# Optimization experiments

Measured on AMD Instinct MI355X. Metric: run time of the kernel, lower is better.

The kernel has to match this reference:

```python
import jax, jax.numpy as jnp
import numpy as np

N, E = 50000, 600000
DIN, DMID, DATTR, DOUT, DEMB, DH, K = 128, 128, 32, 128, 256, 768, 16


def setup_inputs() -> dict:
    key = jax.random.key(0)
    ks = jax.random.split(key, 12)
    s = lambda d: 1.0 / np.sqrt(d)
    return {
        "x": jax.random.normal(ks[0], (N, DIN), jnp.float32),
        "attributes": jax.random.normal(ks[1], (N, DATTR), jnp.float32),
        "edge_weight": jax.random.uniform(ks[2], (E,), jnp.float32),
        "hidden_state": jax.random.normal(ks[3], (1, DH), jnp.float32),
        "edge_index": jax.random.randint(ks[4], (2, E), 0, N, jnp.int64),
        "W1": jax.random.normal(ks[5], (DIN, DMID), jnp.float32) * s(DIN),
        "b1": jnp.zeros((DMID,), jnp.float32),
        "W2": jax.random.normal(ks[6], (DMID + DATTR, DOUT), jnp.float32) * s(DMID + DATTR),
        "b2": jnp.zeros((DOUT,), jnp.float32),
        "Wmap": jax.random.normal(ks[7], (DOUT + DATTR, DEMB), jnp.float32) * s(DOUT + DATTR),
        "bmap": jnp.zeros((DEMB,), jnp.float32),
        "Wattn": jax.random.normal(ks[8], (DH, DOUT + DATTR), jnp.float32) * s(DH),
    }


def gcn_conv(x, W, b, src, dst, w, n):
    """PyG GCNConv with normalize=True: A_hat = D^-1/2 (A+I) D^-1/2, out = A_hat X W + b."""
    loop = jnp.arange(n, dtype=src.dtype)
    src2 = jnp.concatenate([src, loop])
    dst2 = jnp.concatenate([dst, loop])
    w2 = jnp.concatenate([w, jnp.ones((n,), x.dtype)])
    deg = jax.ops.segment_sum(w2, dst2, num_segments=n)
    dinv = jnp.where(deg > 0, jax.lax.rsqrt(jnp.maximum(deg, 1e-12)), 0.0)
    norm = dinv[src2] * w2 * dinv[dst2]        # [E+N]
    h = x @ W                                   # [n, out] transform first (small dim)
    msg = h[src2] * norm[:, None]               # gather + scale, [E+N, out]
    return jax.ops.segment_sum(msg, dst2, num_segments=n) + b


def reference(x, attributes, edge_weight, hidden_state, edge_index,
              W1, b1, W2, b2, Wmap, bmap, Wattn):
    n = x.shape[0]
    src, dst = edge_index[0], edge_index[1]
    h = jax.nn.relu(gcn_conv(x, W1, b1, src, dst, edge_weight, n))
    # F.dropout with training=False is identity (module run in eval mode)
    h = jnp.concatenate([h, attributes], axis=1)           # [N, DMID+DATTR]
    h = gcn_conv(h, W2, b2, src, dst, edge_weight, n)      # [N, DOUT]
    h = jnp.concatenate([h, attributes], axis=1)           # [N, DOUT+DATTR]
    # DotAttnChoseImportentNode: project hidden state, dot with node feats, take top-K nodes
    q = hidden_state @ Wattn                                # [1, DOUT+DATTR]
    scores = h @ q[0]                                       # [N]
    _, idx = jax.lax.top_k(scores, K)
    chose_nodes = h[idx].reshape(1, -1)                     # [1, K*(DOUT+DATTR)]
    # final_mapping: mean-pool graph embed + linear
    emb = jnp.mean(h, axis=0, keepdims=True) @ Wmap + bmap  # [1, DEMB]
    return jnp.concatenate([emb, chose_nodes], axis=1)      # [1, DEMB + K*(DOUT+DATTR)]
```

## Files before the change

kernel.cpp:

```cpp
#include <hip/hip_runtime.h>

#define N_NODES 50000
#define N_EDGES 600000
#define D_IN 128
#define D_MID 128
#define D_ATTR 32
#define D_OUT 128
#define D_EMB 256
#define D_H 768
#define K_TOP 16
#define D_CAT (D_OUT + D_ATTR)
#define N_CHUNKBLKS 196
#define N_CAND (N_CHUNKBLKS * K_TOP)
#define CSLOTS 13
#define WSCALE 262144.0f
#define CS_BLOCKS 768

__global__ void k_init(unsigned long long* packed, float* q) {
    int i = blockIdx.x * blockDim.x + threadIdx.x;
    if (i < N_NODES) packed[i] = 0ULL;
    if (i < D_CAT)   q[i] = 0.0f;
}

__global__ void k_deg(const int* __restrict__ dst, const float* __restrict__ w,
                      unsigned long long* __restrict__ packed) {
    int e = blockIdx.x * blockDim.x + threadIdx.x;
    if (e < N_EDGES) {
        int d = dst[e];
        unsigned long long q = (1ULL << 40)
                             + (unsigned long long)__float2uint_rn(w[e] * WSCALE);
        atomicAdd(&packed[d], q);
    }
}

__global__ void k_dinv(const unsigned long long* __restrict__ packed,
                       float* __restrict__ dinv, int* __restrict__ counts) {
    int i = blockIdx.x * blockDim.x + threadIdx.x;
    if (i < N_NODES) {
        unsigned long long p = packed[i];
        counts[i] = (int)(p >> 40);
        float wsum = (float)(p & 0xFFFFFFFFFFULL) * (1.0f / WSCALE);
        dinv[i] = rsqrtf(1.0f + wsum);
    }
}

__global__ __launch_bounds__(256) void k_scan_blk(const int* __restrict__ counts,
                                                  int* __restrict__ incl,
                                                  int* __restrict__ bsum) {
    __shared__ int sm[256];
    int tid = threadIdx.x;
    int i = blockIdx.x * 256 + tid;
    int v = (i < N_NODES) ? counts[i] : 0;
    sm[tid] = v;
    __syncthreads();
    for (int off = 1; off < 256; off <<= 1) {
        int t = (tid >= off) ? sm[tid - off] : 0;
        __syncthreads();
        sm[tid] += t;
        __syncthreads();
    }
    if (i < N_NODES) incl[i] = sm[tid];
    if (tid == 255) bsum[blockIdx.x] = sm[255];
}

__global__ __launch_bounds__(256) void k_scan_top(const int* __restrict__ bsum,
                                                  int* __restrict__ boff) {
    __shared__ int sm[256];
    int tid = threadIdx.x;
    int v = (tid < N_CHUNKBLKS) ? bsum[tid] : 0;
    sm[tid] = v;
    __syncthreads();
    for (int off = 1; off < 256; off <<= 1) {
        int t = (tid >= off) ? sm[tid - off] : 0;
        __syncthreads();
        sm[tid] += t;
        __syncthreads();
    }
    if (tid < N_CHUNKBLKS) boff[tid] = sm[tid] - v;
}

__global__ __launch_bounds__(256) void k_scan_add(const int* __restrict__ incl,
                                                  const int* __restrict__ boff,
                                                  const int* __restrict__ counts,
                                                  int* __restrict__ row_ptr,
                                                  int* __restrict__ cursor) {
    int i = blockIdx.x * 256 + threadIdx.x;
    if (i < N_NODES) {
        int ip = incl[i] + boff[blockIdx.x];
        row_ptr[i + 1] = ip;
        cursor[i] = ip - counts[i];
        if (i == 0) row_ptr[0] = 0;
    }
}

__global__ void k_fill(const int* __restrict__ src, const int* __restrict__ dst,
                       const float* __restrict__ w, const float* __restrict__ dinv,
                       int* __restrict__ cursor, int2* __restrict__ recs) {
    int e = blockIdx.x * blockDim.x + threadIdx.x;
    if (e < N_EDGES) {
        int s = src[e], d = dst[e];
        int pos = atomicAdd(&cursor[d], 1);
        float nr = dinv[s] * w[e] * dinv[d];
        recs[pos] = make_int2(s, __float_as_int(nr));
    }
}

#define GBM 128
#define GBK 32
__global__ __launch_bounds__(256) void k_gemm(
    const float* __restrict__ in1, int d1,
    const float* __restrict__ in2, int d2,
    const float* __restrict__ W,
    float* __restrict__ out)
{
    __shared__ float xs[GBM][GBK + 1];
    __shared__ float ws[GBK][128];
    int tid = threadIdx.x;
    int cx = tid & 7;
    int ry = tid >> 3;
    int row0 = blockIdx.x * GBM;
    float acc[4][16];
#pragma unroll
    for (int i = 0; i < 4; ++i)
#pragma unroll
        for (int j = 0; j < 16; ++j) acc[i][j] = 0.0f;
    int KD = d1 + d2;
    for (int kt = 0; kt < KD; kt += GBK) {
        const float* srcp; int sd, scol;
        if (kt < d1) { srcp = in1; sd = d1; scol = kt; }
        else         { srcp = in2; sd = d2; scol = kt - d1; }
#pragma unroll
        for (int i = 0; i < 4; ++i) {
            int vid = tid + i * 256;
            int rr = vid >> 3;
            int kc = (vid & 7) * 4;
            int r = row0 + rr;
            float4 val = make_float4(0.f, 0.f, 0.f, 0.f);
            if (r < N_NODES)
                val = *(const float4*)(srcp + (size_t)r * sd + scol + kc);
            xs[rr][kc + 0] = val.x;
            xs[rr][kc + 1] = val.y;
            xs[rr][kc + 2] = val.z;
            xs[rr][kc + 3] = val.w;
        }
#pragma unroll
        for (int i = 0; i < 4; ++i) {
            int vid = tid + i * 256;
            int kk = vid >> 5;
            int c = (vid & 31) * 4;
            *(float4*)&ws[kk][c] = *(const float4*)(W + (size_t)(kt + kk) * 128 + c);
        }
        __syncthreads();
#pragma unroll
        for (int kk = 0; kk < GBK; ++kk) {
            float xv[4];
#pragma unroll
            for (int i = 0; i < 4; ++i) xv[i] = xs[ry * 4 + i][kk];
            float wv[16];
#pragma unroll
            for (int j4 = 0; j4 < 4; ++j4)
                *(float4*)&wv[j4 * 4] = *(float4*)&ws[kk][cx * 4 + j4 * 32];
#pragma unroll
            for (int i = 0; i < 4; ++i)
#pragma unroll
                for (int j = 0; j < 16; ++j)
                    acc[i][j] += xv[i] * wv[j];
        }
        __syncthreads();
    }
#pragma unroll
    for (int i = 0; i < 4; ++i) {
        int r = row0 + ry * 4 + i;
        if (r < N_NODES) {
#pragma unroll
            for (int j4 = 0; j4 < 4; ++j4)
                *(float4*)(out + (size_t)r * 128 + cx * 4 + j4 * 32)
                    = *(float4*)&acc[i][j4 * 4];
        }
    }
}

__global__ __launch_bounds__(256) void k_agg(
    const float* __restrict__ t, const float* __restrict__ dinv,
    const int* __restrict__ row_ptr, const int2* __restrict__ recs,
    const float* __restrict__ bias,
    float* __restrict__ out, int relu_flag,
    const float* __restrict__ attr, const float* __restrict__ q,
    float* __restrict__ scores, int score_flag)
{
    int lane = threadIdx.x & 63;
    int node = blockIdx.x * 4 + (threadIdx.x >> 6);
    if (node >= N_NODES) return;
    const float2* t2 = (const float2*)t;
    float di = dinv[node];
    float sw = di * di;
    float2 v = t2[(size_t)node * 64 + lane];
    float accx = v.x * sw, accy = v.y * sw;
    int e0 = row_ptr[node], e1 = row_ptr[node + 1];
    int len = e1 - e0;
    for (int base = 0; base < len; base += 64) {
        int m = len - base; if (m > 64) m = 64;
        int2 myrec = make_int2(0, 0);
        if (lane < m) myrec = recs[e0 + base + lane];
        int j = 0;
        for (; j + 8 <= m; j += 8) {
            int   s0 = __shfl(myrec.x, j + 0, 64), s1 = __shfl(myrec.x, j + 1, 64);
            int   s2 = __shfl(myrec.x, j + 2, 64), s3 = __shfl(myrec.x, j + 3, 64);
            int   s4 = __shfl(myrec.x, j + 4, 64), s5 = __shfl(myrec.x, j + 5, 64);
            int   s6 = __shfl(myrec.x, j + 6, 64), s7 = __shfl(myrec.x, j + 7, 64);
            float w0 = __int_as_float(__shfl(myrec.y, j + 0, 64));
            float w1 = __int_as_float(__shfl(myrec.y, j + 1, 64));
            float w2 = __int_as_float(__shfl(myrec.y, j + 2, 64));
            float w3 = __int_as_float(__shfl(myrec.y, j + 3, 64));
            float w4 = __int_as_float(__shfl(myrec.y, j + 4, 64));
            float w5 = __int_as_float(__shfl(myrec.y, j + 5, 64));
            float w6 = __int_as_float(__shfl(myrec.y, j + 6, 64));
            float w7 = __int_as_float(__shfl(myrec.y, j + 7, 64));
            float2 u0 = t2[(size_t)s0 * 64 + lane];
            float2 u1 = t2[(size_t)s1 * 64 + lane];
            float2 u2 = t2[(size_t)s2 * 64 + lane];
            float2 u3 = t2[(size_t)s3 * 64 + lane];
            float2 u4 = t2[(size_t)s4 * 64 + lane];
            float2 u5 = t2[(size_t)s5 * 64 + lane];
            float2 u6 = t2[(size_t)s6 * 64 + lane];
            float2 u7 = t2[(size_t)s7 * 64 + lane];
            accx += w0 * u0.x + w1 * u1.x + w2 * u2.x + w3 * u3.x
                  + w4 * u4.x + w5 * u5.x + w6 * u6.x + w7 * u7.x;
            accy += w0 * u0.y + w1 * u1.y + w2 * u2.y + w3 * u3.y
                  + w4 * u4.y + w5 * u5.y + w6 * u6.y + w7 * u7.y;
        }
        for (; j + 4 <= m; j += 4) {
            int s0 = __shfl(myrec.x, j + 0, 64);
            int s1 = __shfl(myrec.x, j + 1, 64);
            int s2 = __shfl(myrec.x, j + 2, 64);
            int s3 = __shfl(myrec.x, j + 3, 64);
            float w0 = __int_as_float(__shfl(myrec.y, j + 0, 64));
            float w1 = __int_as_float(__shfl(myrec.y, j + 1, 64));
            float w2 = __int_as_float(__shfl(myrec.y, j + 2, 64));
            float w3 = __int_as_float(__shfl(myrec.y, j + 3, 64));
            float2 u0 = t2[(size_t)s0 * 64 + lane];
            float2 u1 = t2[(size_t)s1 * 64 + lane];
            float2 u2 = t2[(size_t)s2 * 64 + lane];
            float2 u3 = t2[(size_t)s3 * 64 + lane];
            accx += w0 * u0.x + w1 * u1.x + w2 * u2.x + w3 * u3.x;
            accy += w0 * u0.y + w1 * u1.y + w2 * u2.y + w3 * u3.y;
        }
        for (; j < m; ++j) {
            int s = __shfl(myrec.x, j, 64);
            float wn = __int_as_float(__shfl(myrec.y, j, 64));
            float2 u = t2[(size_t)s * 64 + lane];
            accx += wn * u.x;
            accy += wn * u.y;
        }
    }
    const float2* b2 = (const float2*)bias;
    float2 bb = b2[lane];
    accx += bb.x; accy += bb.y;
    if (relu_flag) {
        accx = fmaxf(accx, 0.0f);
        accy = fmaxf(accy, 0.0f);
    }
    float2 res; res.x = accx; res.y = accy;
    ((float2*)out)[(size_t)node * 64 + lane] = res;
    if (score_flag) {
        const float2* q2 = (const float2*)q;
        float2 qq = q2[lane];
        float s = accx * qq.x + accy * qq.y;
        if (lane < 16) {
            const float2* at2 = (const float2*)attr;
            float2 a = at2[(size_t)node * 16 + lane];
            float2 qa = q2[64 + lane];
            s += a.x * qa.x + a.y * qa.y;
        }
        for (int off = 32; off; off >>= 1) s += __shfl_xor(s, off, 64);
        if (lane == 0) scores[node] = s;
    }
}

__global__ void k_q(const float* __restrict__ hs, const float* __restrict__ Wattn,
                    float* __restrict__ q) {
    int j = threadIdx.x;
    if (j >= D_CAT) return;
    int k0 = blockIdx.x * (D_H / 8);
    float acc = 0.0f;
    for (int k = k0; k < k0 + D_H / 8; k++) acc += hs[k] * Wattn[k * D_CAT + j];
    atomicAdd(&q[j], acc);
}

__global__ __launch_bounds__(256) void k_colsum_partial(const float* __restrict__ h2,
                                                        const float* __restrict__ attr,
                                                        float* __restrict__ partial) {
    __shared__ float4 sm[256];
    int tid = threadIdx.x;
    int per = (N_NODES + CS_BLOCKS - 1) / CS_BLOCKS;
    int r0 = blockIdx.x * per;
    int r1 = min(N_NODES, r0 + per);
    float* myrow = partial + (size_t)blockIdx.x * D_CAT;
    {
        const float4* h4 = (const float4*)h2;
        int c = tid & 31;
        float4 acc = make_float4(0.f, 0.f, 0.f, 0.f);
        for (int r = r0 + (tid >> 5); r < r1; r += 8) {
            float4 v = h4[(size_t)r * 32 + c];
            acc.x += v.x; acc.y += v.y; acc.z += v.z; acc.w += v.w;
        }
        sm[tid] = acc;
        __syncthreads();
        if (tid < 32) {
            float4 s = sm[tid];
#pragma unroll
            for (int g = 1; g < 8; ++g) {
                float4 v = sm[g * 32 + tid];
                s.x += v.x; s.y += v.y; s.z += v.z; s.w += v.w;
            }
            ((float4*)myrow)[tid] = s;
        }
        __syncthreads();
    }
    {
        const float4* a4 = (const float4*)attr;
        int c = tid & 7;
        float4 acc = make_float4(0.f, 0.f, 0.f, 0.f);
        for (int r = r0 + (tid >> 3); r < r1; r += 32) {
            float4 v = a4[(size_t)r * 8 + c];
            acc.x += v.x; acc.y += v.y; acc.z += v.z; acc.w += v.w;
        }
        sm[tid] = acc;
        __syncthreads();
        if (tid < 8) {
            float4 s = sm[tid];
#pragma unroll
            for (int g = 1; g < 32; ++g) {
                float4 v = sm[g * 8 + tid];
                s.x += v.x; s.y += v.y; s.z += v.z; s.w += v.w;
            }
            ((float4*)(myrow + D_OUT))[tid] = s;
        }
    }
}

__global__ __launch_bounds__(256) void k_colsum_reduce(const float* __restrict__ partial,
                                                       float* __restrict__ colsum) {
    __shared__ float4 sm[256];
    int tid = threadIdx.x;
    int cg = blockIdx.x;
    float4 acc = make_float4(0.f, 0.f, 0.f, 0.f);
#pragma unroll
    for (int k = 0; k < 3; ++k) {
        int b = tid + k * 256;
        float4 v = *(const float4*)(partial + (size_t)b * D_CAT + cg * 4);
        acc.x += v.x; acc.y += v.y; acc.z += v.z; acc.w += v.w;
    }
    sm[tid] = acc;
    __syncthreads();
    for (int off = 128; off; off >>= 1) {
        if (tid < off) {
            float4 v = sm[tid + off];
            sm[tid].x += v.x; sm[tid].y += v.y; sm[tid].z += v.z; sm[tid].w += v.w;
        }
        __syncthreads();
    }
    if (tid == 0) *(float4*)(colsum + cg * 4) = sm[0];
}

__global__ __launch_bounds__(256) void k_top1(const float* __restrict__ scores,
                                              float* __restrict__ cand_s,
                                              int* __restrict__ cand_i) {
    __shared__ float ss[256];
    __shared__ int si[256];
    __shared__ float rs[256];
    __shared__ int ri[256];
    int tid = threadIdx.x;
    int i = blockIdx.x * 256 + tid;
    ss[tid] = (i < N_NODES) ? scores[i] : -INFINITY;
    si[tid] = i;
    __syncthreads();
    for (int it = 0; it < K_TOP; ++it) {
        rs[tid] = ss[tid]; ri[tid] = si[tid];
        __syncthreads();
        for (int off = 128; off; off >>= 1) {
            if (tid < off) {
                float s2 = rs[tid + off]; int i2 = ri[tid + off];
                if (s2 > rs[tid] || (s2 == rs[tid] && i2 < ri[tid])) { rs[tid] = s2; ri[tid] = i2; }
            }
            __syncthreads();
        }
        if (tid == 0) {
            cand_s[blockIdx.x * K_TOP + it] = rs[0];
            cand_i[blockIdx.x * K_TOP + it] = ri[0];
        }
        __syncthreads();
        if (si[tid] == ri[0]) ss[tid] = -INFINITY;
        __syncthreads();
    }
}

__global__ __launch_bounds__(256) void k_top2(const float* __restrict__ cand_s,
                                              const int* __restrict__ cand_i,
                                              int* __restrict__ topidx) {
    float s[CSLOTS]; int ix[CSLOTS];
    int tid = threadIdx.x;
    int lane = tid & 63;
    int wave = tid >> 6;
#pragma unroll
    for (int j = 0; j < CSLOTS; ++j) {
        int c = tid + j * 256;
        s[j]  = (c < N_CAND) ? cand_s[c] : -INFINITY;
        ix[j] = (c < N_CAND) ? cand_i[c] : 0x7fffffff;
    }
    __shared__ float wsum_s[4];
    __shared__ int   wsum_i[4];
    __shared__ int   win_i;
    for (int it = 0; it < K_TOP; ++it) {
        float bs = -INFINITY; int bi = 0x7fffffff;
#pragma unroll
        for (int j = 0; j < CSLOTS; ++j) {
            if (s[j] > bs || (s[j] == bs && ix[j] < bi)) { bs = s[j]; bi = ix[j]; }
        }
#pragma unroll
        for (int off = 32; off; off >>= 1) {
            float s2 = __shfl_xor(bs, off, 64);
            int   i2 = __shfl_xor(bi, off, 64);
            if (s2 > bs || (s2 == bs && i2 < bi)) { bs = s2; bi = i2; }
        }
        if (lane == 0) { wsum_s[wave] = bs; wsum_i[wave] = bi; }
        __syncthreads();
        if (tid == 0) {
            float ws0 = wsum_s[0]; int wi0 = wsum_i[0];
#pragma unroll
            for (int w = 1; w < 4; ++w) {
                float s2 = wsum_s[w]; int i2 = wsum_i[w];
                if (s2 > ws0 || (s2 == ws0 && i2 < wi0)) { ws0 = s2; wi0 = i2; }
            }
            win_i = wi0;
            topidx[it] = wi0;
        }
        __syncthreads();
        int w = win_i;
#pragma unroll
        for (int j = 0; j < CSLOTS; ++j)
            if (ix[j] == w) s[j] = -INFINITY;
        __syncthreads();
    }
}

__global__ __launch_bounds__(256) void k_emb_gather(
    const float* __restrict__ colsum, const float* __restrict__ Wmap,
    const float* __restrict__ bmap, const int* __restrict__ topidx,
    const float* __restrict__ h2, const float* __restrict__ attr,
    float* __restrict__ out)
{
    int tid = threadIdx.x;
    __shared__ float cs[D_CAT];
    if (tid < D_CAT) cs[tid] = colsum[tid];
    __syncthreads();
    float acc = 0.0f;
#pragma unroll 8
    for (int k = 0; k < D_CAT; ++k) acc += cs[k] * Wmap[k * D_EMB + tid];
    out[tid] = acc * (1.0f / N_NODES) + bmap[tid];
    __shared__ int ti[K_TOP];
    if (tid < K_TOP) ti[tid] = topidx[tid];
    __syncthreads();
    for (int idx = tid; idx < K_TOP * D_CAT; idx += 256) {
        int kk = idx / D_CAT;
        int d = idx % D_CAT;
        int node = ti[kk];
        out[D_EMB + idx] = (d < D_OUT) ? h2[node * D_OUT + d]
                                       : attr[node * D_ATTR + (d - D_OUT)];
    }
}

extern "C" void kernel_launch(void* const* d_in, const int* in_sizes, int n_in,
                              void* d_out, int out_size, void* d_ws, size_t ws_size,
                              hipStream_t stream) {
    const float* x      = (const float*)d_in[0];
    const float* attr   = (const float*)d_in[1];
    const float* ew     = (const float*)d_in[2];
    const float* hs     = (const float*)d_in[3];
    const int*   ei     = (const int*)d_in[4];
    const float* W1     = (const float*)d_in[5];
    const float* b1     = (const float*)d_in[6];
    const float* W2     = (const float*)d_in[7];
    const float* b2     = (const float*)d_in[8];
    const float* Wmap   = (const float*)d_in[9];
    const float* bmap   = (const float*)d_in[10];
    const float* Wattn  = (const float*)d_in[11];
    float* out = (float*)d_out;
    const int* e_src = ei;
    const int* e_dst = ei + N_EDGES;

    size_t off = 0;
    auto alloc = [&](size_t bytes) {
        void* p = (char*)d_ws + off;
        off += (bytes + 255) / 256 * 256;
        return p;
    };
    unsigned long long* packed = (unsigned long long*)alloc((size_t)N_NODES * 8);
    float* dinv   = (float*)alloc((size_t)N_NODES * 4);
    int*   counts = (int*)  alloc((size_t)N_NODES * 4);
    int*   rowp   = (int*)  alloc((size_t)(N_NODES + 1) * 4);
    int*   cursor = (int*)  alloc((size_t)N_NODES * 4);
    int2*  recs   = (int2*) alloc((size_t)N_EDGES * 8);
    float* bufA   = (float*)alloc((size_t)N_NODES * 128 * 4);
    float* bufB   = (float*)alloc((size_t)N_NODES * 128 * 4);
    float* scores = (float*)alloc((size_t)N_NODES * 4);
    float* q      = (float*)alloc(D_CAT * 4);
    float* colsum = (float*)alloc(D_CAT * 4);
    float* partial= (float*)alloc((size_t)CS_BLOCKS * D_CAT * 4);
    float* cand_s = (float*)alloc((size_t)N_CAND * 4);
    int*   cand_i = (int*)  alloc((size_t)N_CAND * 4);
    int*   incl   = (int*)  alloc((size_t)N_NODES * 4);
    int*   bsum   = (int*)  alloc((size_t)N_CHUNKBLKS * 4);
    int*   boff   = (int*)  alloc((size_t)N_CHUNKBLKS * 4);
    int*   topidx = (int*)  alloc((size_t)K_TOP * 4);

    int nblk = (N_NODES + 255) / 256;
    int eblk = (N_EDGES + 255) / 256;

    hipLaunchKernelGGL(k_init, dim3(nblk), dim3(256), 0, stream, packed, q);
    hipLaunchKernelGGL(k_deg, dim3(eblk), dim3(256), 0, stream, e_dst, ew, packed);
    hipLaunchKernelGGL(k_dinv, dim3(nblk), dim3(256), 0, stream, packed, dinv, counts);
    hipLaunchKernelGGL(k_scan_blk, dim3(nblk), dim3(256), 0, stream, counts, incl, bsum);
    hipLaunchKernelGGL(k_scan_top, dim3(1), dim3(256), 0, stream, bsum, boff);
    hipLaunchKernelGGL(k_scan_add, dim3(nblk), dim3(256), 0, stream, incl, boff, counts,
                       rowp, cursor);
    hipLaunchKernelGGL(k_fill, dim3(eblk), dim3(256), 0, stream, e_src, e_dst, ew, dinv,
                       cursor, recs);
    hipLaunchKernelGGL(k_q, dim3(8), dim3(192), 0, stream, hs, Wattn, q);
    hipLaunchKernelGGL(k_gemm, dim3((N_NODES + GBM - 1) / GBM), dim3(256), 0, stream,
                       x, D_IN, x, 0, W1, bufA);
    hipLaunchKernelGGL(k_agg, dim3((N_NODES + 3) / 4), dim3(256), 0, stream,
                       bufA, dinv, rowp, recs, b1, bufB, 1,
                       (const float*)nullptr, (const float*)nullptr, (float*)nullptr, 0);
    hipLaunchKernelGGL(k_gemm, dim3((N_NODES + GBM - 1) / GBM), dim3(256), 0, stream,
                       bufB, D_MID, attr, D_ATTR, W2, bufA);
    hipLaunchKernelGGL(k_agg, dim3((N_NODES + 3) / 4), dim3(256), 0, stream,
                       bufA, dinv, rowp, recs, b2, bufB, 0,
                       attr, q, scores, 1);
    hipLaunchKernelGGL(k_colsum_partial, dim3(CS_BLOCKS), dim3(256), 0, stream,
                       bufB, attr, partial);
    hipLaunchKernelGGL(k_colsum_reduce, dim3(D_CAT / 4), dim3(256), 0, stream,
                       partial, colsum);
    hipLaunchKernelGGL(k_top1, dim3(N_CHUNKBLKS), dim3(256), 0, stream,
                       scores, cand_s, cand_i);
    hipLaunchKernelGGL(k_top2, dim3(1), dim3(256), 0, stream, cand_s, cand_i, topidx);
    hipLaunchKernelGGL(k_emb_gather, dim3(1), dim3(256), 0, stream,
                       colsum, Wmap, bmap, topidx, bufB, attr, out);
}
```

Measured before the change: 308.4 us.

## Fuse dinv into scan, shrink GEMM tile, wave-shuffle top-k, merge top2 with emb

Folds the dinv/count extraction into the block scan and reads counts from the packed word, which removes one kernel and the counts buffer. The GEMM row tile drops from 128 to 64 rows per block, doubling the grid and lowering register use per thread. The per-block top-16 selection now uses wave shuffles plus a 4-entry shared-memory reduction instead of a full shared-memory tree with many barriers. The final top-k merge and the embedding/gather kernel are combined into one launch, which removes a tiny launch and the topidx round trip.

Measured after the change: 302.5 us. No clear change (-1.9%).

```diff
diff --git a/kernel.cpp b/kernel.cpp
--- a/kernel.cpp
+++ b/kernel.cpp
@@ -33,24 +33,19 @@
     }
 }
 
-__global__ void k_dinv(const unsigned long long* __restrict__ packed,
-                       float* __restrict__ dinv, int* __restrict__ counts) {
-    int i = blockIdx.x * blockDim.x + threadIdx.x;
-    if (i < N_NODES) {
-        unsigned long long p = packed[i];
-        counts[i] = (int)(p >> 40);
-        float wsum = (float)(p & 0xFFFFFFFFFFULL) * (1.0f / WSCALE);
-        dinv[i] = rsqrtf(1.0f + wsum);
-    }
-}
-
-__global__ __launch_bounds__(256) void k_scan_blk(const int* __restrict__ counts,
+__global__ __launch_bounds__(256) void k_scan_blk(const unsigned long long* __restrict__ packed,
+                                                  float* __restrict__ dinv,
                                                   int* __restrict__ incl,
                                                   int* __restrict__ bsum) {
     __shared__ int sm[256];
     int tid = threadIdx.x;
     int i = blockIdx.x * 256 + tid;
-    int v = (i < N_NODES) ? counts[i] : 0;
+    unsigned long long p = (i < N_NODES) ? packed[i] : 0ULL;
+    int v = (int)(p >> 40);
+    if (i < N_NODES) {
+        float wsum = (float)(p & 0xFFFFFFFFFFULL) * (1.0f / WSCALE);
+        dinv[i] = rsqrtf(1.0f + wsum);
+    }
     sm[tid] = v;
     __syncthreads();
     for (int off = 1; off < 256; off <<= 1) {
@@ -81,14 +76,14 @@
 
 __global__ __launch_bounds__(256) void k_scan_add(const int* __restrict__ incl,
                                                   const int* __restrict__ boff,
-                                                  const int* __restrict__ counts,
+                                                  const unsigned long long* __restrict__ packed,
                                                   int* __restrict__ row_ptr,
                                                   int* __restrict__ cursor) {
     int i = blockIdx.x * 256 + threadIdx.x;
     if (i < N_NODES) {
         int ip = incl[i] + boff[blockIdx.x];
         row_ptr[i + 1] = ip;
-        cursor[i] = ip - counts[i];
+        cursor[i] = ip - (int)(packed[i] >> 40);
         if (i == 0) row_ptr[0] = 0;
     }
 }
@@ -105,7 +100,7 @@
     }
 }
 
-#define GBM 128
+#define GBM 64
 #define GBK 32
 __global__ __launch_bounds__(256) void k_gemm(
     const float* __restrict__ in1, int d1,
@@ -119,9 +114,9 @@
     int cx = tid & 7;
     int ry = tid >> 3;
     int row0 = blockIdx.x * GBM;
-    float acc[4][16];
-#pragma unroll
-    for (int i = 0; i < 4; ++i)
+    float acc[2][16];
+#pragma unroll
+    for (int i = 0; i < 2; ++i)
 #pragma unroll
         for (int j = 0; j < 16; ++j) acc[i][j] = 0.0f;
     int KD = d1 + d2;
@@ -130,7 +125,7 @@
         if (kt < d1) { srcp = in1; sd = d1; scol = kt; }
         else         { srcp = in2; sd = d2; scol = kt - d1; }
 #pragma unroll
-        for (int i = 0; i < 4; ++i) {
+        for (int i = 0; i < 2; ++i) {
             int vid = tid + i * 256;
             int rr = vid >> 3;
             int kc = (vid & 7) * 4;
@@ -153,24 +148,23 @@
         __syncthreads();
 #pragma unroll
         for (int kk = 0; kk < GBK; ++kk) {
-            float xv[4];
-#pragma unroll
-            for (int i = 0; i < 4; ++i) xv[i] = xs[ry * 4 + i][kk];
+            float xv0 = xs[ry * 2 + 0][kk];
+            float xv1 = xs[ry * 2 + 1][kk];
             float wv[16];
 #pragma unroll
             for (int j4 = 0; j4 < 4; ++j4)
                 *(float4*)&wv[j4 * 4] = *(float4*)&ws[kk][cx * 4 + j4 * 32];
 #pragma unroll
-            for (int i = 0; i < 4; ++i)
-#pragma unroll
-                for (int j = 0; j < 16; ++j)
-                    acc[i][j] += xv[i] * wv[j];
-        }
-        __syncthreads();
-    }
-#pragma unroll
-    for (int i = 0; i < 4; ++i) {
-        int r = row0 + ry * 4 + i;
+            for (int j = 0; j < 16; ++j) {
+                acc[0][j] += xv0 * wv[j];
+                acc[1][j] += xv1 * wv[j];
+            }
+        }
+        __syncthreads();
+    }
+#pragma unroll
+    for (int i = 0; i < 2; ++i) {
+        int r = row0 + ry * 2 + i;
         if (r < N_NODES) {
 #pragma unroll
             for (int j4 = 0; j4 < 4; ++j4)
@@ -366,38 +360,46 @@
 __global__ __launch_bounds__(256) void k_top1(const float* __restrict__ scores,
                                               float* __restrict__ cand_s,
                                               int* __restrict__ cand_i) {
-    __shared__ float ss[256];
-    __shared__ int si[256];
-    __shared__ float rs[256];
-    __shared__ int ri[256];
-    int tid = threadIdx.x;
+    int tid = threadIdx.x;
+    int lane = tid & 63;
+    int wave = tid >> 6;
     int i = blockIdx.x * 256 + tid;
-    ss[tid] = (i < N_NODES) ? scores[i] : -INFINITY;
-    si[tid] = i;
-    __syncthreads();
+    float s = (i < N_NODES) ? scores[i] : -INFINITY;
+    int ix = i;
+    __shared__ float wls[4];
+    __shared__ int   wli[4];
+    __shared__ int   fin_i;
     for (int it = 0; it < K_TOP; ++it) {
-        rs[tid] = ss[tid]; ri[tid] = si[tid];
-        __syncthreads();
-        for (int off = 128; off; off >>= 1) {
-            if (tid < off) {
-                float s2 = rs[tid + off]; int i2 = ri[tid + off];
-                if (s2 > rs[tid] || (s2 == rs[tid] && i2 < ri[tid])) { rs[tid] = s2; ri[tid] = i2; }
-            }
-            __syncthreads();
-        }
+        float bs = s; int bi = ix;
+#pragma unroll
+        for (int off = 32; off; off >>= 1) {
+            float s2 = __shfl_xor(bs, off, 64);
+            int   i2 = __shfl_xor(bi, off, 64);
+            if (s2 > bs || (s2 == bs && i2 < bi)) { bs = s2; bi = i2; }
+        }
+        if (lane == 0) { wls[wave] = bs; wli[wave] = bi; }
+        __syncthreads();
         if (tid == 0) {
-            cand_s[blockIdx.x * K_TOP + it] = rs[0];
-            cand_i[blockIdx.x * K_TOP + it] = ri[0];
-        }
-        __syncthreads();
-        if (si[tid] == ri[0]) ss[tid] = -INFINITY;
-        __syncthreads();
-    }
-}
-
-__global__ __launch_bounds__(256) void k_top2(const float* __restrict__ cand_s,
-                                              const int* __restrict__ cand_i,
-                                              int* __restrict__ topidx) {
+            float f = wls[0]; int fi = wli[0];
+#pragma unroll
+            for (int w = 1; w < 4; ++w)
+                if (wls[w] > f || (wls[w] == f && wli[w] < fi)) { f = wls[w]; fi = wli[w]; }
+            cand_s[blockIdx.x * K_TOP + it] = f;
+            cand_i[blockIdx.x * K_TOP + it] = fi;
+            fin_i = fi;
+        }
+        __syncthreads();
+        if (ix == fin_i) s = -INFINITY;
+    }
+}
+
+__global__ __launch_bounds__(256) void k_top2emb(
+    const float* __restrict__ cand_s, const int* __restrict__ cand_i,
+    const float* __restrict__ colsum, const float* __restrict__ Wmap,
+    const float* __restrict__ bmap,
+    const float* __restrict__ h2, const float* __restrict__ attr,
+    float* __restrict__ out)
+{
     float s[CSLOTS]; int ix[CSLOTS];
     int tid = threadIdx.x;
     int lane = tid & 63;
@@ -411,6 +413,7 @@
     __shared__ float wsum_s[4];
     __shared__ int   wsum_i[4];
     __shared__ int   win_i;
+    __shared__ int   ti[K_TOP];
     for (int it = 0; it < K_TOP; ++it) {
         float bs = -INFINITY; int bi = 0x7fffffff;
 #pragma unroll
@@ -433,7 +436,7 @@
                 if (s2 > ws0 || (s2 == ws0 && i2 < wi0)) { ws0 = s2; wi0 = i2; }
             }
             win_i = wi0;
-            topidx[it] = wi0;
+            ti[it] = wi0;
         }
         __syncthreads();
         int w = win_i;
@@ -442,15 +445,6 @@
             if (ix[j] == w) s[j] = -INFINITY;
         __syncthreads();
     }
-}
-
-__global__ __launch_bounds__(256) void k_emb_gather(
-    const float* __restrict__ colsum, const float* __restrict__ Wmap,
-    const float* __restrict__ bmap, const int* __restrict__ topidx,
-    const float* __restrict__ h2, const float* __restrict__ attr,
-    float* __restrict__ out)
-{
-    int tid = threadIdx.x;
     __shared__ float cs[D_CAT];
     if (tid < D_CAT) cs[tid] = colsum[tid];
     __syncthreads();
@@ -458,9 +452,6 @@
 #pragma unroll 8
     for (int k = 0; k < D_CAT; ++k) acc += cs[k] * Wmap[k * D_EMB + tid];
     out[tid] = acc * (1.0f / N_NODES) + bmap[tid];
-    __shared__ int ti[K_TOP];
-    if (tid < K_TOP) ti[tid] = topidx[tid];
-    __syncthreads();
     for (int idx = tid; idx < K_TOP * D_CAT; idx += 256) {
         int kk = idx / D_CAT;
         int d = idx % D_CAT;
@@ -497,7 +488,6 @@
     };
     unsigned long long* packed = (unsigned long long*)alloc((size_t)N_NODES * 8);
     float* dinv   = (float*)alloc((size_t)N_NODES * 4);
-    int*   counts = (int*)  alloc((size_t)N_NODES * 4);
     int*   rowp   = (int*)  alloc((size_t)(N_NODES + 1) * 4);
     int*   cursor = (int*)  alloc((size_t)N_NODES * 4);
     int2*  recs   = (int2*) alloc((size_t)N_EDGES * 8);
@@ -512,17 +502,15 @@
     int*   incl   = (int*)  alloc((size_t)N_NODES * 4);
     int*   bsum   = (int*)  alloc((size_t)N_CHUNKBLKS * 4);
     int*   boff   = (int*)  alloc((size_t)N_CHUNKBLKS * 4);
-    int*   topidx = (int*)  alloc((size_t)K_TOP * 4);
 
     int nblk = (N_NODES + 255) / 256;
     int eblk = (N_EDGES + 255) / 256;
 
     hipLaunchKernelGGL(k_init, dim3(nblk), dim3(256), 0, stream, packed, q);
     hipLaunchKernelGGL(k_deg, dim3(eblk), dim3(256), 0, stream, e_dst, ew, packed);
-    hipLaunchKernelGGL(k_dinv, dim3(nblk), dim3(256), 0, stream, packed, dinv, counts);
-    hipLaunchKernelGGL(k_scan_blk, dim3(nblk), dim3(256), 0, stream, counts, incl, bsum);
+    hipLaunchKernelGGL(k_scan_blk, dim3(nblk), dim3(256), 0, stream, packed, dinv, incl, bsum);
     hipLaunchKernelGGL(k_scan_top, dim3(1), dim3(256), 0, stream, bsum, boff);
-    hipLaunchKernelGGL(k_scan_add, dim3(nblk), dim3(256), 0, stream, incl, boff, counts,
+    hipLaunchKernelGGL(k_scan_add, dim3(nblk), dim3(256), 0, stream, incl, boff, packed,
                        rowp, cursor);
     hipLaunchKernelGGL(k_fill, dim3(eblk), dim3(256), 0, stream, e_src, e_dst, ew, dinv,
                        cursor, recs);
@@ -543,7 +531,6 @@
                        partial, colsum);
     hipLaunchKernelGGL(k_top1, dim3(N_CHUNKBLKS), dim3(256), 0, stream,
                        scores, cand_s, cand_i);
-    hipLaunchKernelGGL(k_top2, dim3(1), dim3(256), 0, stream, cand_s, cand_i, topidx);
-    hipLaunchKernelGGL(k_emb_gather, dim3(1), dim3(256), 0, stream,
-                       colsum, Wmap, bmap, topidx, bufB, attr, out);
-}
+    hipLaunchKernelGGL(k_top2emb, dim3(1), dim3(256), 0, stream,
+                       cand_s, cand_i, colsum, Wmap, bmap, bufB, attr, out);
+}
```
